# Performance work log

Measured on AMD Instinct MI355X. Metric: run time of the kernel, lower is better.

Reference implementation:

```python
import jax, jax.numpy as jnp
import numpy as np

B, K, F, C = 256, 16, 128, 2
EPS = 1e-5


def setup_inputs() -> dict:
    key = jax.random.key(0)
    ks = jax.random.split(key, 16)
    n = lambda k, shape, s=1.0: (jax.random.normal(k, shape, dtype=jnp.float32) * s)
    return {
        "x0": n(ks[0], (B, F)),
        "x1": n(ks[1], (B, K, F)),
        "x2": n(ks[2], (B, K * K, F)),
        "x3": n(ks[3], (B, K ** 3, F)),
        "W0": n(ks[4], (2 * F, F), 0.05), "b0": n(ks[5], (F,), 0.05),
        "W1": n(ks[6], (2 * F, F), 0.05), "b1": n(ks[7], (F,), 0.05),
        "W2": n(ks[8], (2 * F, F), 0.05), "b2": n(ks[9], (F,), 0.05),
        "lin1_W": n(ks[10], (F, 8), 0.05), "lin1_b": n(ks[11], (8,), 0.05),
        "bn_gamma": jnp.ones((8,), jnp.float32), "bn_beta": jnp.zeros((8,), jnp.float32),
        "lin2_W": n(ks[12], (8, C), 0.05), "lin2_b": n(ks[13], (C,), 0.05),
    }


def _agg_mean(x):
    # block-wise mean over groups of K along dim 1: [B, N, F] -> [B, N//K, F]
    b, n_, f = x.shape
    return x.reshape(b, n_ // K, K, f).mean(axis=2)


def reference(x0, x1, x2, x3, W0, b0, W1, b1, W2, b2,
              lin1_W, lin1_b, bn_gamma, bn_beta, lin2_W, lin2_b):
    # layer i=3: mean-agg x3 blocks, concat with x2, Linear(2F->F)+ReLU
    h2 = jax.nn.relu(jnp.concatenate([_agg_mean(x3), x2], axis=2) @ W2 + b2)
    # layer i=2
    h1 = jax.nn.relu(jnp.concatenate([_agg_mean(h2), x1], axis=2) @ W1 + b1)
    # layer i=1: agg gives [B,1,F]; squeeze and concat along feature dim
    h0 = jax.nn.relu(jnp.concatenate([_agg_mean(h1)[:, 0, :], x0], axis=1) @ W0 + b0)
    # classifier head: Linear -> BatchNorm1d (training batch stats) -> Linear -> Sigmoid
    z = h0 @ lin1_W + lin1_b                       # [B, 8]
    mu = z.mean(axis=0)
    var = jnp.mean(jnp.square(z - mu), axis=0)     # biased var, as torch BN
    zn = (z - mu) * jax.lax.rsqrt(var + EPS) * bn_gamma + bn_beta
    return jax.nn.sigmoid(zn @ lin2_W + lin2_b)    # [B, C]
```

## Files before the change

### kernel.cpp

```cpp
#include <hip/hip_runtime.h>
#include <math.h>

#define F_DIM 128
#define TM 64
#define NTHR 256

__global__ __launch_bounds__(NTHR, 2)
void layer_kernel(const float* __restrict__ deep,
                  const float* __restrict__ shallow,
                  const float* __restrict__ W,
                  const float* __restrict__ bias,
                  float* __restrict__ out)
{
    __shared__ float A[TM * 256];
    const int t  = threadIdx.x;
    const int m0 = blockIdx.x * TM;

    {
        const int r8 = t >> 5;
        const int l  = t & 31;
        const int fo = l * 4;
        for (int rr = r8; rr < TM; rr += 8) {
            const int m = m0 + rr;
            const float4* dp = (const float4*)(deep + (size_t)m * 2048 + fo);
            float4 s = dp[0];
            #pragma unroll
            for (int k = 1; k < 16; ++k) {
                float4 v = dp[k * 32];
                s.x += v.x; s.y += v.y; s.z += v.z; s.w += v.w;
            }
            const float inv = 1.0f / 16.0f;
            float4 sh = *(const float4*)(shallow + (size_t)m * F_DIM + fo);
            const int sw = rr * 4;
            *(float4*)(&A[rr * 256 + ((fo + sw) & 255)]) =
                make_float4(s.x * inv, s.y * inv, s.z * inv, s.w * inv);
            *(float4*)(&A[rr * 256 + ((128 + fo + sw) & 255)]) = sh;
        }
    }
    __syncthreads();

    const int ty = t >> 4;
    const int tx = t & 15;
    float acc[4][8];
    #pragma unroll
    for (int i = 0; i < 4; ++i)
        #pragma unroll
        for (int j = 0; j < 8; ++j) acc[i][j] = 0.0f;

    const float* Wp = W + tx * 8;
    for (int kk = 0; kk < 256; kk += 4) {
        float4 a[4];
        #pragma unroll
        for (int i = 0; i < 4; ++i) {
            const int r = ty * 4 + i;
            a[i] = *(const float4*)(&A[r * 256 + ((kk + r * 4) & 255)]);
        }
        float4 w0[4], w1[4];
        #pragma unroll
        for (int d = 0; d < 4; ++d) {
            const float* wr = Wp + (kk + d) * F_DIM;
            w0[d] = *(const float4*)(wr);
            w1[d] = *(const float4*)(wr + 4);
        }
        #pragma unroll
        for (int i = 0; i < 4; ++i) {
            const float av0 = a[i].x, av1 = a[i].y, av2 = a[i].z, av3 = a[i].w;
            acc[i][0] += av0*w0[0].x + av1*w0[1].x + av2*w0[2].x + av3*w0[3].x;
            acc[i][1] += av0*w0[0].y + av1*w0[1].y + av2*w0[2].y + av3*w0[3].y;
            acc[i][2] += av0*w0[0].z + av1*w0[1].z + av2*w0[2].z + av3*w0[3].z;
            acc[i][3] += av0*w0[0].w + av1*w0[1].w + av2*w0[2].w + av3*w0[3].w;
            acc[i][4] += av0*w1[0].x + av1*w1[1].x + av2*w1[2].x + av3*w1[3].x;
            acc[i][5] += av0*w1[0].y + av1*w1[1].y + av2*w1[2].y + av3*w1[3].y;
            acc[i][6] += av0*w1[0].z + av1*w1[1].z + av2*w1[2].z + av3*w1[3].z;
            acc[i][7] += av0*w1[0].w + av1*w1[1].w + av2*w1[2].w + av3*w1[3].w;
        }
    }

    const float4 b0 = *(const float4*)(bias + tx * 8);
    const float4 b1 = *(const float4*)(bias + tx * 8 + 4);
    #pragma unroll
    for (int i = 0; i < 4; ++i) {
        const int m = m0 + ty * 4 + i;
        float4 o0 = make_float4(fmaxf(acc[i][0] + b0.x, 0.0f),
                                fmaxf(acc[i][1] + b0.y, 0.0f),
                                fmaxf(acc[i][2] + b0.z, 0.0f),
                                fmaxf(acc[i][3] + b0.w, 0.0f));
        float4 o1 = make_float4(fmaxf(acc[i][4] + b1.x, 0.0f),
                                fmaxf(acc[i][5] + b1.y, 0.0f),
                                fmaxf(acc[i][6] + b1.z, 0.0f),
                                fmaxf(acc[i][7] + b1.w, 0.0f));
        float* op = out + (size_t)m * F_DIM + tx * 8;
        *(float4*)op       = o0;
        *(float4*)(op + 4) = o1;
    }
}

__global__ __launch_bounds__(NTHR)
void head_kernel(const float* __restrict__ h0,
                 const float* __restrict__ l1W,
                 const float* __restrict__ l1b,
                 const float* __restrict__ gamma,
                 const float* __restrict__ beta,
                 const float* __restrict__ l2W,
                 const float* __restrict__ l2b,
                 float* __restrict__ out)
{
    __shared__ float z[256][8];
    __shared__ float w1s[128 * 8];
    __shared__ float ps[32][8];
    __shared__ float pq[32][8];
    __shared__ float scale_s[8], shift_s[8];

    const int t  = threadIdx.x;
    const int j  = t & 7;
    const int rg = t >> 3;

    #pragma unroll
    for (int i = 0; i < 4; ++i) w1s[t * 4 + i] = l1W[t * 4 + i];
    __syncthreads();

    const float bj = l1b[j];
    for (int it = 0; it < 8; ++it) {
        const int b = it * 32 + rg;
        const float4* hr = (const float4*)(h0 + (size_t)b * 128);
        float s = bj;
        #pragma unroll
        for (int f4 = 0; f4 < 32; ++f4) {
            float4 h = hr[f4];
            s += h.x * w1s[(f4 * 4 + 0) * 8 + j];
            s += h.y * w1s[(f4 * 4 + 1) * 8 + j];
            s += h.z * w1s[(f4 * 4 + 2) * 8 + j];
            s += h.w * w1s[(f4 * 4 + 3) * 8 + j];
        }
        z[b][j] = s;
    }
    __syncthreads();

    {
        float s = 0.0f, q = 0.0f;
        #pragma unroll
        for (int r = 0; r < 8; ++r) {
            float v = z[rg * 8 + r][j];
            s += v; q += v * v;
        }
        ps[rg][j] = s; pq[rg][j] = q;
    }
    __syncthreads();

    if (t < 8) {
        float s = 0.0f, q = 0.0f;
        #pragma unroll
        for (int p = 0; p < 32; ++p) { s += ps[p][t]; q += pq[p][t]; }
        const float mu  = s * (1.0f / 256.0f);
        const float var = q * (1.0f / 256.0f) - mu * mu;
        const float sc  = gamma[t] * rsqrtf(var + 1e-5f);
        scale_s[t] = sc;
        shift_s[t] = beta[t] - mu * sc;
    }
    __syncthreads();

    {
        float o0 = l2b[0], o1 = l2b[1];
        #pragma unroll
        for (int jj = 0; jj < 8; ++jj) {
            const float zn = z[t][jj] * scale_s[jj] + shift_s[jj];
            o0 += zn * l2W[jj * 2 + 0];
            o1 += zn * l2W[jj * 2 + 1];
        }
        out[t * 2 + 0] = 1.0f / (1.0f + expf(-o0));
        out[t * 2 + 1] = 1.0f / (1.0f + expf(-o1));
    }
}

extern "C" void kernel_launch(void* const* d_in, const int* in_sizes, int n_in,
                              void* d_out, int out_size, void* d_ws, size_t ws_size,
                              hipStream_t stream)
{
    const float* x0    = (const float*)d_in[0];
    const float* x1    = (const float*)d_in[1];
    const float* x2    = (const float*)d_in[2];
    const float* x3    = (const float*)d_in[3];
    const float* W0    = (const float*)d_in[4];
    const float* b0    = (const float*)d_in[5];
    const float* W1    = (const float*)d_in[6];
    const float* b1    = (const float*)d_in[7];
    const float* W2    = (const float*)d_in[8];
    const float* b2    = (const float*)d_in[9];
    const float* l1W   = (const float*)d_in[10];
    const float* l1b   = (const float*)d_in[11];
    const float* gamma = (const float*)d_in[12];
    const float* beta  = (const float*)d_in[13];
    const float* l2W   = (const float*)d_in[14];
    const float* l2b   = (const float*)d_in[15];
    float* out = (float*)d_out;

    float* h2 = (float*)d_ws;
    float* h1 = h2 + (size_t)256 * 256 * 128;
    float* h0 = h1 + (size_t)256 * 16 * 128;

    hipLaunchKernelGGL(layer_kernel, dim3(65536 / TM), dim3(NTHR), 0, stream,
                       x3, x2, W2, b2, h2);
    hipLaunchKernelGGL(layer_kernel, dim3(4096 / TM), dim3(NTHR), 0, stream,
                       h2, x1, W1, b1, h1);
    hipLaunchKernelGGL(layer_kernel, dim3(256 / TM), dim3(NTHR), 0, stream,
                       h1, x0, W0, b0, h0);
    hipLaunchKernelGGL(head_kernel, dim3(1), dim3(NTHR), 0, stream,
                       h0, l1W, l1b, gamma, beta, l2W, l2b, out);
}
```

Before: 886.4 us.

## Store LDS activation tile as bf16 and template tile height per layer

The shared-memory activation tile is now held as bf16 (rounded on store, widened on load) with a padded row stride in place of the XOR-style swizzle. This halves LDS use so launch bounds can target four blocks per SM. The tile height is now a template parameter, so the smaller layers launch more blocks. The cost is bf16 rounding of the inputs to the GEMM, which adds error, plus extra unpack instructions in the inner loop.

```diff
diff --git a/kernel.cpp b/kernel.cpp
--- a/kernel.cpp
+++ b/kernel.cpp
@@ -1,18 +1,26 @@
 #include <hip/hip_runtime.h>
 #include <math.h>
 
-#define F_DIM 128
-#define TM 64
 #define NTHR 256
 
-__global__ __launch_bounds__(NTHR, 2)
+__device__ __forceinline__ unsigned short f2bf(float x) {
+    unsigned int u = __float_as_uint(x);
+    return (unsigned short)((u + 0x7fffu + ((u >> 16) & 1u)) >> 16);
+}
+__device__ __forceinline__ ushort4 pack4(float a, float b, float c, float d) {
+    return make_ushort4(f2bf(a), f2bf(b), f2bf(c), f2bf(d));
+}
+
+template<int TM>
+__global__ __launch_bounds__(NTHR, 4)
 void layer_kernel(const float* __restrict__ deep,
                   const float* __restrict__ shallow,
                   const float* __restrict__ W,
                   const float* __restrict__ bias,
                   float* __restrict__ out)
 {
-    __shared__ float A[TM * 256];
+    constexpr int RP = TM / 16;
+    __shared__ unsigned short A[TM][264];
     const int t  = threadIdx.x;
     const int m0 = blockIdx.x * TM;
 
@@ -30,57 +38,59 @@
                 s.x += v.x; s.y += v.y; s.z += v.z; s.w += v.w;
             }
             const float inv = 1.0f / 16.0f;
-            float4 sh = *(const float4*)(shallow + (size_t)m * F_DIM + fo);
-            const int sw = rr * 4;
-            *(float4*)(&A[rr * 256 + ((fo + sw) & 255)]) =
-                make_float4(s.x * inv, s.y * inv, s.z * inv, s.w * inv);
-            *(float4*)(&A[rr * 256 + ((128 + fo + sw) & 255)]) = sh;
+            float4 sh = *(const float4*)(shallow + (size_t)m * 128 + fo);
+            *(ushort4*)&A[rr][fo]       = pack4(s.x * inv, s.y * inv, s.z * inv, s.w * inv);
+            *(ushort4*)&A[rr][128 + fo] = pack4(sh.x, sh.y, sh.z, sh.w);
         }
     }
     __syncthreads();
 
     const int ty = t >> 4;
     const int tx = t & 15;
-    float acc[4][8];
+    float acc[RP][8];
     #pragma unroll
-    for (int i = 0; i < 4; ++i)
+    for (int i = 0; i < RP; ++i)
         #pragma unroll
         for (int j = 0; j < 8; ++j) acc[i][j] = 0.0f;
 
     const float* Wp = W + tx * 8;
     for (int kk = 0; kk < 256; kk += 4) {
-        float4 a[4];
-        #pragma unroll
-        for (int i = 0; i < 4; ++i) {
-            const int r = ty * 4 + i;
-            a[i] = *(const float4*)(&A[r * 256 + ((kk + r * 4) & 255)]);
+        float av[RP][4];
+        #pragma unroll
+        for (int i = 0; i < RP; ++i) {
+            const int r = ty * RP + i;
+            uint2 q = *(const uint2*)&A[r][kk];
+            av[i][0] = __uint_as_float(q.x << 16);
+            av[i][1] = __uint_as_float(q.x & 0xffff0000u);
+            av[i][2] = __uint_as_float(q.y << 16);
+            av[i][3] = __uint_as_float(q.y & 0xffff0000u);
         }
         float4 w0[4], w1[4];
         #pragma unroll
         for (int d = 0; d < 4; ++d) {
-            const float* wr = Wp + (kk + d) * F_DIM;
+            const float* wr = Wp + (kk + d) * 128;
             w0[d] = *(const float4*)(wr);
             w1[d] = *(const float4*)(wr + 4);
         }
         #pragma unroll
-        for (int i = 0; i < 4; ++i) {
-            const float av0 = a[i].x, av1 = a[i].y, av2 = a[i].z, av3 = a[i].w;
-            acc[i][0] += av0*w0[0].x + av1*w0[1].x + av2*w0[2].x + av3*w0[3].x;
-            acc[i][1] += av0*w0[0].y + av1*w0[1].y + av2*w0[2].y + av3*w0[3].y;
-            acc[i][2] += av0*w0[0].z + av1*w0[1].z + av2*w0[2].z + av3*w0[3].z;
-            acc[i][3] += av0*w0[0].w + av1*w0[1].w + av2*w0[2].w + av3*w0[3].w;
-            acc[i][4] += av0*w1[0].x + av1*w1[1].x + av2*w1[2].x + av3*w1[3].x;
-            acc[i][5] += av0*w1[0].y + av1*w1[1].y + av2*w1[2].y + av3*w1[3].y;
-            acc[i][6] += av0*w1[0].z + av1*w1[1].z + av2*w1[2].z + av3*w1[3].z;
-            acc[i][7] += av0*w1[0].w + av1*w1[1].w + av2*w1[2].w + av3*w1[3].w;
+        for (int i = 0; i < RP; ++i) {
+            const float a0 = av[i][0], a1 = av[i][1], a2 = av[i][2], a3 = av[i][3];
+            acc[i][0] += a0*w0[0].x + a1*w0[1].x + a2*w0[2].x + a3*w0[3].x;
+            acc[i][1] += a0*w0[0].y + a1*w0[1].y + a2*w0[2].y + a3*w0[3].y;
+            acc[i][2] += a0*w0[0].z + a1*w0[1].z + a2*w0[2].z + a3*w0[3].z;
+            acc[i][3] += a0*w0[0].w + a1*w0[1].w + a2*w0[2].w + a3*w0[3].w;
+            acc[i][4] += a0*w1[0].x + a1*w1[1].x + a2*w1[2].x + a3*w1[3].x;
+            acc[i][5] += a0*w1[0].y + a1*w1[1].y + a2*w1[2].y + a3*w1[3].y;
+            acc[i][6] += a0*w1[0].z + a1*w1[1].z + a2*w1[2].z + a3*w1[3].z;
+            acc[i][7] += a0*w1[0].w + a1*w1[1].w + a2*w1[2].w + a3*w1[3].w;
         }
     }
 
     const float4 b0 = *(const float4*)(bias + tx * 8);
     const float4 b1 = *(const float4*)(bias + tx * 8 + 4);
     #pragma unroll
-    for (int i = 0; i < 4; ++i) {
-        const int m = m0 + ty * 4 + i;
+    for (int i = 0; i < RP; ++i) {
+        const int m = m0 + ty * RP + i;
         float4 o0 = make_float4(fmaxf(acc[i][0] + b0.x, 0.0f),
                                 fmaxf(acc[i][1] + b0.y, 0.0f),
                                 fmaxf(acc[i][2] + b0.z, 0.0f),
@@ -89,7 +99,7 @@
                                 fmaxf(acc[i][5] + b1.y, 0.0f),
                                 fmaxf(acc[i][6] + b1.z, 0.0f),
                                 fmaxf(acc[i][7] + b1.w, 0.0f));
-        float* op = out + (size_t)m * F_DIM + tx * 8;
+        float* op = out + (size_t)m * 128 + tx * 8;
         *(float4*)op       = o0;
         *(float4*)(op + 4) = o1;
     }
@@ -195,14 +205,14 @@
     float* out = (float*)d_out;
 
     float* h2 = (float*)d_ws;
-    float* h1 = h2 + (size_t)256 * 256 * 128;
-    float* h0 = h1 + (size_t)256 * 16 * 128;
-
-    hipLaunchKernelGGL(layer_kernel, dim3(65536 / TM), dim3(NTHR), 0, stream,
+    float* h1 = h2 + (size_t)65536 * 128;
+    float* h0 = h1 + (size_t)4096 * 128;
+
+    hipLaunchKernelGGL((layer_kernel<64>), dim3(65536 / 64), dim3(NTHR), 0, stream,
                        x3, x2, W2, b2, h2);
-    hipLaunchKernelGGL(layer_kernel, dim3(4096 / TM), dim3(NTHR), 0, stream,
+    hipLaunchKernelGGL((layer_kernel<32>), dim3(4096 / 32), dim3(NTHR), 0, stream,
                        h2, x1, W1, b1, h1);
-    hipLaunchKernelGGL(layer_kernel, dim3(256 / TM), dim3(NTHR), 0, stream,
+    hipLaunchKernelGGL((layer_kernel<16>), dim3(256 / 16), dim3(NTHR), 0, stream,
                        h1, x0, W0, b0, h0);
     hipLaunchKernelGGL(head_kernel, dim3(1), dim3(NTHR), 0, stream,
                        h0, l1W, l1b, gamma, beta, l2W, l2b, out);
```

Result: slower. 905.3 us (+2.1%).
